# Performance work log

Hardware: AMD Instinct MI355X
Metric: run time of the kernel (lower is better)

Reference implementation:

```python
import jax, jax.numpy as jnp
import numpy as np

B, I, H = 16384, 512, 512


def _linear_params(key, out_dim, in_dim):
    kw, kb = jax.random.split(key)
    bound = 1.0 / np.sqrt(in_dim)
    W = jax.random.uniform(kw, (out_dim, in_dim), jnp.float32, -bound, bound)
    b = jax.random.uniform(kb, (out_dim,), jnp.float32, -bound, bound)
    return W, b


def setup_inputs() -> dict:
    key = jax.random.key(0)
    ks = jax.random.split(key, 12)
    x = jax.random.normal(ks[0], (B, I), jnp.float32)
    h_prev = jax.random.normal(ks[1], (B, H), jnp.float32)
    c_prev = jax.random.normal(ks[2], (B, H), jnp.float32)
    W_xi, b_xi = _linear_params(ks[3], H, I)
    W_hi, b_hi = _linear_params(ks[4], H, H)
    W_xf, b_xf = _linear_params(ks[5], H, I)
    W_hf, b_hf = _linear_params(ks[6], H, H)
    W_xc, b_xc = _linear_params(ks[7], H, I)
    W_hc, b_hc = _linear_params(ks[8], H, H)
    W_xo, b_xo = _linear_params(ks[9], H, I)
    W_ho, b_ho = _linear_params(ks[10], H, H)
    W_e, b_e = _linear_params(ks[11], H, I + H)
    return dict(x=x, h_prev=h_prev, c_prev=c_prev,
                W_xi=W_xi, b_xi=b_xi, W_hi=W_hi, b_hi=b_hi,
                W_xf=W_xf, b_xf=b_xf, W_hf=W_hf, b_hf=b_hf,
                W_xc=W_xc, b_xc=b_xc, W_hc=W_hc, b_hc=b_hc,
                W_xo=W_xo, b_xo=b_xo, W_ho=W_ho, b_ho=b_ho,
                W_e=W_e, b_e=b_e)


def reference(x, h_prev, c_prev,
              W_xi, b_xi, W_hi, b_hi,
              W_xf, b_xf, W_hf, b_hf,
              W_xc, b_xc, W_hc, b_hc,
              W_xo, b_xo, W_ho, b_ho,
              W_e, b_e):
    # Batch the 4 input-to-hidden projections into one GEMM and the 4
    # hidden-to-hidden projections into another (same math as 8 Linears).
    Wx = jnp.concatenate([W_xi, W_xf, W_xc, W_xo], axis=0)   # [4H, I]
    bx = jnp.concatenate([b_xi, b_xf, b_xc, b_xo], axis=0)   # [4H]
    Wh = jnp.concatenate([W_hi, W_hf, W_hc, W_ho], axis=0)   # [4H, H]
    bh = jnp.concatenate([b_hi, b_hf, b_hc, b_ho], axis=0)
    gates = (x @ Wx.T + bx) + (h_prev @ Wh.T + bh)            # [B, 4H]
    gi, gf, gc, go = jnp.split(gates, 4, axis=-1)
    i = jax.nn.sigmoid(gi)
    f = jax.nn.sigmoid(gf)
    g = jnp.tanh(gc)
    o = jax.nn.sigmoid(go)
    c = f * c_prev + i * g
    # exp gate: Linear on [x, h_prev] -> tanh -> exp; split W_e to avoid concat
    We_x, We_h = W_e[:, :x.shape[-1]], W_e[:, x.shape[-1]:]
    exp_factor = jnp.exp(jnp.tanh(x @ We_x.T + h_prev @ We_h.T + b_e))
    h = o * jnp.tanh(c) * exp_factor
    return (h, c)
```

## Files before the change

### kernel.cpp

```cpp
#include <hip/hip_runtime.h>
#include <stdint.h>

#define Bsz 16384
#define Hh  512
#define Kd  1024
#define BM  128
#define BNJ 32
#define BK  64
#define NT  16

#define LDSB 36864

typedef __attribute__((ext_vector_type(8))) short bf16x8;
typedef __attribute__((ext_vector_type(4))) float f32x4;
typedef __attribute__((ext_vector_type(8))) unsigned short u16x8;

__device__ __forceinline__ unsigned short f2bf(float f) {
    union { float f; unsigned u; } v; v.f = f;
    unsigned u = v.u;
    return (unsigned short)((u + 0x7fffu + ((u >> 16) & 1u)) >> 16);
}
__device__ __forceinline__ float fast_tanh(float x) {
    float e = __expf(2.f * x);
    return (e - 1.f) / (e + 1.f);
}
__device__ __forceinline__ float fast_sigmoid(float x) {
    return 1.f / (1.f + __expf(-x));
}

__global__ void pack_A(const float* __restrict__ x, const float* __restrict__ h,
                       unsigned short* __restrict__ A) {
    const long total = (long)Bsz * Kd / 8;
    for (long i = (long)blockIdx.x * blockDim.x + threadIdx.x; i < total;
         i += (long)gridDim.x * blockDim.x) {
        long row = i >> 7;
        int  col = ((int)(i & 127)) << 3;
        const float* src = (col < 512) ? (x + row * 512 + col)
                                       : (h + row * 512 + (col - 512));
        float4 f0 = *(const float4*)(src);
        float4 f1 = *(const float4*)(src + 4);
        u16x8 o;
        o[0]=f2bf(f0.x); o[1]=f2bf(f0.y); o[2]=f2bf(f0.z); o[3]=f2bf(f0.w);
        o[4]=f2bf(f1.x); o[5]=f2bf(f1.y); o[6]=f2bf(f1.z); o[7]=f2bf(f1.w);
        *(u16x8*)(A + (i << 3)) = o;
    }
}

__global__ void pack_B(const float* __restrict__ Wxi, const float* __restrict__ Whi,
                       const float* __restrict__ Wxf, const float* __restrict__ Whf,
                       const float* __restrict__ Wxc, const float* __restrict__ Whc,
                       const float* __restrict__ Wxo, const float* __restrict__ Who,
                       const float* __restrict__ We,
                       const float* __restrict__ bxi, const float* __restrict__ bhi,
                       const float* __restrict__ bxf, const float* __restrict__ bhf,
                       const float* __restrict__ bxc, const float* __restrict__ bhc,
                       const float* __restrict__ bxo, const float* __restrict__ bho,
                       const float* __restrict__ be,
                       unsigned short* __restrict__ Bp, float* __restrict__ bias) {
    const long id = (long)blockIdx.x * blockDim.x + threadIdx.x;
    if (id < 327680) {
        int blk = (int)(id >> 6);
        int l   = (int)(id & 63);
        int kh  = blk & 1;
        int kt  = (blk >> 1) & 15;
        int rest = blk >> 5;
        int g    = rest % 5;
        int jgrp = rest / 5;
        int j  = jgrp * 16 + (l & 15);
        int k0 = kt * 64 + kh * 32 + ((l >> 4) << 3);
        const float* src;
        if (g == 4) {
            src = We + (long)j * 1024 + k0;
        } else {
            const float* Wx = (g == 0) ? Wxi : (g == 1) ? Wxf : (g == 2) ? Wxc : Wxo;
            const float* Wh = (g == 0) ? Whi : (g == 1) ? Whf : (g == 2) ? Whc : Who;
            src = (k0 < 512) ? (Wx + (long)j * 512 + k0)
                             : (Wh + (long)j * 512 + (k0 - 512));
        }
        float4 f0 = *(const float4*)(src);
        float4 f1 = *(const float4*)(src + 4);
        u16x8 o;
        o[0]=f2bf(f0.x); o[1]=f2bf(f0.y); o[2]=f2bf(f0.z); o[3]=f2bf(f0.w);
        o[4]=f2bf(f1.x); o[5]=f2bf(f1.y); o[6]=f2bf(f1.z); o[7]=f2bf(f1.w);
        *(u16x8*)(Bp + (long)blk * 512 + l * 8) = o;
    }
    if (id < 2560) {
        int row = (int)id;
        int g = row >> 9, j = row & 511;
        float b;
        if (g == 4) b = be[j];
        else {
            const float* bx = (g == 0) ? bxi : (g == 1) ? bxf : (g == 2) ? bxc : bxo;
            const float* bh = (g == 0) ? bhi : (g == 1) ? bhf : (g == 2) ? bhc : bho;
            b = bx[j] + bh[j];
        }
        bias[row] = b;
    }
}

#define GL16(g, l) __builtin_amdgcn_global_load_lds( \
    (const __attribute__((address_space(1))) unsigned int*)(g), \
    (__attribute__((address_space(3))) unsigned int*)(l), 16, 0, 0)

#define WAITVM0()  asm volatile("s_waitcnt vmcnt(0)" ::: "memory")
#define LGKM_I(n)  asm volatile("s_waitcnt lgkmcnt(" #n ")" ::: "memory")
#define LGKM(n)    LGKM_I(n)
#define BARRIER()  asm volatile("s_barrier" ::: "memory")
#define SCHED0()   __builtin_amdgcn_sched_barrier(0)

#define MF(a, b, c) __builtin_amdgcn_mfma_f32_16x16x32_bf16(a, b, c, 0, 0, 0)

#define RDA(KH, APTR) do { \
    afA[KH][0] = *(const bf16x8*)((APTR) + 0 * 2048); \
    afA[KH][1] = *(const bf16x8*)((APTR) + 1 * 2048); \
    afA[KH][2] = *(const bf16x8*)((APTR) + 2 * 2048); \
    afA[KH][3] = *(const bf16x8*)((APTR) + 3 * 2048); \
} while (0)

#define RDB(SET, BPTR, KH) do { \
    SET[0] = *(const bf16x8*)((BPTR) + (0 + (KH)) * 1024); \
    SET[1] = *(const bf16x8*)((BPTR) + (2 + (KH)) * 1024); \
    SET[2] = *(const bf16x8*)((BPTR) + (4 + (KH)) * 1024); \
    SET[3] = *(const bf16x8*)((BPTR) + (6 + (KH)) * 1024); \
    SET[4] = *(const bf16x8*)((BPTR) + (8 + (KH)) * 1024); \
} while (0)

#define SGA(SO, T) do { \
    GL16(asrc + 0 * 32768 + (T) * 64, lds_raw + (SO) + adst + 0 * 4096); \
    GL16(asrc + 1 * 32768 + (T) * 64, lds_raw + (SO) + adst + 1 * 4096); \
    GL16(asrc + 2 * 32768 + (T) * 64, lds_raw + (SO) + adst + 2 * 4096); \
    GL16(asrc + 3 * 32768 + (T) * 64, lds_raw + (SO) + adst + 3 * 4096); \
} while (0)

#define SGB(SO, T) do { \
    GL16(bsg0 + (T) * 1024, lds_raw + (SO) + bdo0); \
    GL16(bsg1 + (T) * 1024, lds_raw + (SO) + bdo1); \
    GL16(bsg2 + (T) * 1024, lds_raw + (SO) + bdo2); \
    GL16(bsg3 + (T) * 1024, lds_raw + (SO) + bdo3); \
    GL16(bsg4 + (T) * 1024, lds_raw + (SO) + bdo4); \
} while (0)

#define MFMA20(KH, BSET) do { \
    __builtin_amdgcn_s_setprio(1); \
    _Pragma("unroll") \
    for (int g_ = 0; g_ < 5; ++g_) { \
        acc[g_][0] = MF(afA[KH][0], BSET[g_], acc[g_][0]); \
        acc[g_][1] = MF(afA[KH][1], BSET[g_], acc[g_][1]); \
        acc[g_][2] = MF(afA[KH][2], BSET[g_], acc[g_][2]); \
        acc[g_][3] = MF(afA[KH][3], BSET[g_], acc[g_][3]); \
    } \
    __builtin_amdgcn_s_setprio(0); \
} while (0)

#define TILE(AP0, AP1, BPTR, SO, T, STG, SYNC) do { \
    if (STG) { SGB(SO, (T) + 1); SGA(SO, (T) + 1); } SCHED0(); \
    RDA(0, AP0); RDB(bq0, BPTR, 0); SCHED0(); \
    RDA(1, AP1); RDB(bq1, BPTR, 1); SCHED0(); \
    LGKM(9); SCHED0(); \
    MFMA20(0, bq0); SCHED0(); \
    LGKM(0); SCHED0(); \
    MFMA20(1, bq1); \
    if (SYNC) { WAITVM0(); BARRIER(); } \
} while (0)

__global__ __launch_bounds__(256, 2)
void xlstm_gemm(const unsigned short* __restrict__ A,
                const unsigned short* __restrict__ Bp,
                const float* __restrict__ bias,
                const float* __restrict__ c_prev,
                float* __restrict__ out) {
    __shared__ __align__(16) unsigned char lds_raw[2 * LDSB];

    const int tid  = threadIdx.x;
    const int wid  = tid >> 6;
    const int lane = tid & 63;
    const int wm   = wid >> 1;
    const int wj   = wid & 1;
    const int fr   = lane & 15;
    const int q    = lane >> 4;

    const int orig = blockIdx.x;
    const int wg   = (orig & 7) * 256 + (orig >> 3);
    const int mblk = wg >> 4;
    const int jblk = wg & 15;
    const long brow = (long)mblk * BM;
    const int  bcol = jblk * BNJ;

    f32x4 acc[5][4];
#pragma unroll
    for (int g = 0; g < 5; ++g)
#pragma unroll
        for (int m = 0; m < 4; ++m)
#pragma unroll
            for (int r = 0; r < 4; ++r) acc[g][m][r] = 0.f;

    bf16x8 afA[2][4];
    bf16x8 bq0[5], bq1[5];

    const int aboff = (wm * 64 + fr) * 128;
    const int swz0  = ((q) ^ (fr & 7)) << 4;
    const int swz1  = ((4 | q) ^ (fr & 7)) << 4;
    const unsigned char* aP0k0 = lds_raw + aboff + swz0;
    const unsigned char* aP0k1 = lds_raw + aboff + swz1;
    const unsigned char* aP1k0 = aP0k0 + LDSB;
    const unsigned char* aP1k1 = aP0k1 + LDSB;
    const unsigned char* bP0 = lds_raw + 16384 + wj * 10240 + lane * 16;
    const unsigned char* bP1 = bP0 + LDSB;

    const int r0_ = tid >> 3;
    const unsigned short* asrc = A + (brow + r0_) * 1024L
                                   + (((tid & 7) ^ (r0_ & 7)) << 3);
    const int adst = tid * 16;
    const int f0_ = tid >> 6;
    const unsigned short *bsg0, *bsg1, *bsg2, *bsg3, *bsg4;
    int bdo0, bdo1, bdo2, bdo3, bdo4;
#define BSTG_INIT(i) do { \
    int f_ = f0_ + 4 * (i); int jl_ = f_ / 10; int rem_ = f_ - 10 * jl_; \
    bsg##i = Bp + (long)(jblk * 2 + jl_) * 81920 + (rem_ >> 1) * 16384 \
               + (rem_ & 1) * 512 + (tid & 63) * 8; \
    bdo##i = 16384 + jl_ * 10240 + rem_ * 1024 + (tid & 63) * 16; \
} while (0)
    BSTG_INIT(0); BSTG_INIT(1); BSTG_INIT(2); BSTG_INIT(3); BSTG_INIT(4);

    SGB(0, 0);
    SGA(0, 0);
    WAITVM0();
    BARRIER();

    for (int t = 0; t < 14; t += 2) {
        TILE(aP0k0, aP0k1, bP0, LDSB, t,     1, 1);
        TILE(aP1k0, aP1k1, bP1, 0,    t + 1, 1, 1);
    }
    TILE(aP0k0, aP0k1, bP0, LDSB, 14, 1, 1);
    TILE(aP1k0, aP1k1, bP1, 0,    15, 0, 0);

    const int j = bcol + wj * 16 + fr;
    const float bi_ = bias[j];
    const float bf_ = bias[512 + j];
    const float bc_ = bias[1024 + j];
    const float bo_ = bias[1536 + j];
    const float be_ = bias[2048 + j];
    const long mbase = brow + wm * 64 + (q << 2);
#pragma unroll
    for (int m = 0; m < 4; ++m) {
#pragma unroll
        for (int r = 0; r < 4; ++r) {
            long row = mbase + m * 16 + r;
            float gi = acc[0][m][r] + bi_;
            float gf = acc[1][m][r] + bf_;
            float gc = acc[2][m][r] + bc_;
            float go = acc[3][m][r] + bo_;
            float ge = acc[4][m][r] + be_;
            float iv = fast_sigmoid(gi);
            float fv = fast_sigmoid(gf);
            float gv = fast_tanh(gc);
            float ov = fast_sigmoid(go);
            float ef = __expf(fast_tanh(ge));
            float cp = c_prev[row * 512 + j];
            float cv = fv * cp + iv * gv;
            float hv = ov * fast_tanh(cv) * ef;
            out[row * 512 + j] = hv;
            out[(long)Bsz * 512 + row * 512 + j] = cv;
        }
    }
}

extern "C" void kernel_launch(void* const* d_in, const int* in_sizes, int n_in,
                              void* d_out, int out_size, void* d_ws, size_t ws_size,
                              hipStream_t stream) {
    const float* x      = (const float*)d_in[0];
    const float* h_prev = (const float*)d_in[1];
    const float* c_prev = (const float*)d_in[2];
    const float* Wxi = (const float*)d_in[3];
    const float* bxi = (const float*)d_in[4];
    const float* Whi = (const float*)d_in[5];
    const float* bhi = (const float*)d_in[6];
    const float* Wxf = (const float*)d_in[7];
    const float* bxf = (const float*)d_in[8];
    const float* Whf = (const float*)d_in[9];
    const float* bhf = (const float*)d_in[10];
    const float* Wxc = (const float*)d_in[11];
    const float* bxc = (const float*)d_in[12];
    const float* Whc = (const float*)d_in[13];
    const float* bhc = (const float*)d_in[14];
    const float* Wxo = (const float*)d_in[15];
    const float* bxo = (const float*)d_in[16];
    const float* Who = (const float*)d_in[17];
    const float* bho = (const float*)d_in[18];
    const float* We  = (const float*)d_in[19];
    const float* be  = (const float*)d_in[20];

    unsigned short* Abf  = (unsigned short*)d_ws;
    unsigned short* Bp   = (unsigned short*)((char*)d_ws + 33554432);
    float*          bias = (float*)((char*)d_ws + 33554432 + 5242880);

    pack_A<<<2048, 256, 0, stream>>>(x, h_prev, Abf);
    pack_B<<<1280, 256, 0, stream>>>(Wxi, Whi, Wxf, Whf, Wxc, Whc, Wxo, Who, We,
                                     bxi, bhi, bxf, bhf, bxc, bhc, bxo, bho, be,
                                     Bp, bias);
    xlstm_gemm<<<2048, 256, 0, stream>>>(Abf, Bp, bias, c_prev, (float*)d_out);
}
```

Measured before the change: 124.0 us.

## Restructure GEMM into 8-wave blocks with 4-buffer BK=32 LDS pipeline

The GEMM kernel now uses 512 threads per block (8 waves, each covering 32 rows instead of 64) with BK halved to 32, and a 4-stage LDS ring buffer in place of double buffering. Global-to-LDS loads are issued three tiles ahead with partial vmcnt waits, and LDS fragment reads for the next tile are double-buffered in registers so they overlap the current MFMAs. The aim is to hide memory latency and raise wave occupancy. In exchange there are twice as many barriers, and each wave does less MFMA work between syncs.

```diff
diff --git a/kernel.cpp b/kernel.cpp
--- a/kernel.cpp
+++ b/kernel.cpp
@@ -6,10 +6,10 @@
 #define Kd  1024
 #define BM  128
 #define BNJ 32
-#define BK  64
-#define NT  16
-
-#define LDSB 36864
+#define BK  32
+#define NT  32
+
+#define BUFB 18432
 
 typedef __attribute__((ext_vector_type(8))) short bf16x8;
 typedef __attribute__((ext_vector_type(4))) float f32x4;
@@ -102,7 +102,8 @@
     (const __attribute__((address_space(1))) unsigned int*)(g), \
     (__attribute__((address_space(3))) unsigned int*)(l), 16, 0, 0)
 
-#define WAITVM0()  asm volatile("s_waitcnt vmcnt(0)" ::: "memory")
+#define VM_I(n)    asm volatile("s_waitcnt vmcnt(" #n ")" ::: "memory")
+#define VM(n)      VM_I(n)
 #define LGKM_I(n)  asm volatile("s_waitcnt lgkmcnt(" #n ")" ::: "memory")
 #define LGKM(n)    LGKM_I(n)
 #define BARRIER()  asm volatile("s_barrier" ::: "memory")
@@ -110,66 +111,67 @@
 
 #define MF(a, b, c) __builtin_amdgcn_mfma_f32_16x16x32_bf16(a, b, c, 0, 0, 0)
 
-#define RDA(KH, APTR) do { \
-    afA[KH][0] = *(const bf16x8*)((APTR) + 0 * 2048); \
-    afA[KH][1] = *(const bf16x8*)((APTR) + 1 * 2048); \
-    afA[KH][2] = *(const bf16x8*)((APTR) + 2 * 2048); \
-    afA[KH][3] = *(const bf16x8*)((APTR) + 3 * 2048); \
-} while (0)
-
-#define RDB(SET, BPTR, KH) do { \
-    SET[0] = *(const bf16x8*)((BPTR) + (0 + (KH)) * 1024); \
-    SET[1] = *(const bf16x8*)((BPTR) + (2 + (KH)) * 1024); \
-    SET[2] = *(const bf16x8*)((BPTR) + (4 + (KH)) * 1024); \
-    SET[3] = *(const bf16x8*)((BPTR) + (6 + (KH)) * 1024); \
-    SET[4] = *(const bf16x8*)((BPTR) + (8 + (KH)) * 1024); \
-} while (0)
-
-#define SGA(SO, T) do { \
-    GL16(asrc + 0 * 32768 + (T) * 64, lds_raw + (SO) + adst + 0 * 4096); \
-    GL16(asrc + 1 * 32768 + (T) * 64, lds_raw + (SO) + adst + 1 * 4096); \
-    GL16(asrc + 2 * 32768 + (T) * 64, lds_raw + (SO) + adst + 2 * 4096); \
-    GL16(asrc + 3 * 32768 + (T) * 64, lds_raw + (SO) + adst + 3 * 4096); \
-} while (0)
-
-#define SGB(SO, T) do { \
-    GL16(bsg0 + (T) * 1024, lds_raw + (SO) + bdo0); \
-    GL16(bsg1 + (T) * 1024, lds_raw + (SO) + bdo1); \
-    GL16(bsg2 + (T) * 1024, lds_raw + (SO) + bdo2); \
-    GL16(bsg3 + (T) * 1024, lds_raw + (SO) + bdo3); \
-    GL16(bsg4 + (T) * 1024, lds_raw + (SO) + bdo4); \
-} while (0)
-
-#define MFMA20(KH, BSET) do { \
+#define RD7(S, BO) do { \
+    q##S##0 = *(const bf16x8*)(bP + (BO) + 0 * 1024); \
+    q##S##1 = *(const bf16x8*)(bP + (BO) + 1 * 1024); \
+    q##S##2 = *(const bf16x8*)(bP + (BO) + 2 * 1024); \
+    q##S##3 = *(const bf16x8*)(bP + (BO) + 3 * 1024); \
+    q##S##4 = *(const bf16x8*)(bP + (BO) + 4 * 1024); \
+    a##S##0 = *(const bf16x8*)(aP + (BO) + 0 * 1024); \
+    a##S##1 = *(const bf16x8*)(aP + (BO) + 1 * 1024); \
+} while (0)
+
+#define MFMA10(S) do { \
     __builtin_amdgcn_s_setprio(1); \
-    _Pragma("unroll") \
-    for (int g_ = 0; g_ < 5; ++g_) { \
-        acc[g_][0] = MF(afA[KH][0], BSET[g_], acc[g_][0]); \
-        acc[g_][1] = MF(afA[KH][1], BSET[g_], acc[g_][1]); \
-        acc[g_][2] = MF(afA[KH][2], BSET[g_], acc[g_][2]); \
-        acc[g_][3] = MF(afA[KH][3], BSET[g_], acc[g_][3]); \
+    acc[0][0] = MF(a##S##0, q##S##0, acc[0][0]); \
+    acc[0][1] = MF(a##S##1, q##S##0, acc[0][1]); \
+    acc[1][0] = MF(a##S##0, q##S##1, acc[1][0]); \
+    acc[1][1] = MF(a##S##1, q##S##1, acc[1][1]); \
+    acc[2][0] = MF(a##S##0, q##S##2, acc[2][0]); \
+    acc[2][1] = MF(a##S##1, q##S##2, acc[2][1]); \
+    acc[3][0] = MF(a##S##0, q##S##3, acc[3][0]); \
+    acc[3][1] = MF(a##S##1, q##S##3, acc[3][1]); \
+    acc[4][0] = MF(a##S##0, q##S##4, acc[4][0]); \
+    acc[4][1] = MF(a##S##1, q##S##4, acc[4][1]); \
+    __builtin_amdgcn_s_setprio(0); \
+} while (0)
+
+#define SG3(BO, T) do { \
+    GL16(sg0 + (long)(T) * st0, lds_raw + (BO) + sd0); \
+    GL16(sg1 + (long)(T) * st1, lds_raw + (BO) + sd1); \
+    GL16(sg2 + (long)(T) * st2, lds_raw + (BO) + sd2); \
+} while (0)
+
+#define TILE_F(T, SC, SN, RBO, SBO, STG, SYNC, WN) do { \
+    if (STG) SG3(SBO, (T) + 3); \
+    RD7(SN, RBO); \
+    LGKM(7); SCHED0(); \
+    MFMA10(SC); \
+    if (SYNC) { VM(WN); BARRIER(); } \
+} while (0)
+
+#define SLOT_INIT(i) do { \
+    int u_ = wid * 3 + (i); if (u_ >= 18) u_ -= 18; \
+    if (u_ < 8) { \
+        int row_ = u_ * 16 + (lane >> 2); \
+        sg##i = A + (brow + row_) * 1024L \
+                  + (((lane & 3) ^ ((row_ >> 1) & 3)) << 3); \
+        st##i = 32; \
+    } else { \
+        int b_ = u_ - 8; int jl_ = b_ / 5; int g_ = b_ - 5 * jl_; \
+        sg##i = Bp + (long)(jblk * 2 + jl_) * 81920 + g_ * 16384 + lane * 8; \
+        st##i = 512; \
     } \
-    __builtin_amdgcn_s_setprio(0); \
-} while (0)
-
-#define TILE(AP0, AP1, BPTR, SO, T, STG, SYNC) do { \
-    if (STG) { SGB(SO, (T) + 1); SGA(SO, (T) + 1); } SCHED0(); \
-    RDA(0, AP0); RDB(bq0, BPTR, 0); SCHED0(); \
-    RDA(1, AP1); RDB(bq1, BPTR, 1); SCHED0(); \
-    LGKM(9); SCHED0(); \
-    MFMA20(0, bq0); SCHED0(); \
-    LGKM(0); SCHED0(); \
-    MFMA20(1, bq1); \
-    if (SYNC) { WAITVM0(); BARRIER(); } \
-} while (0)
-
-__global__ __launch_bounds__(256, 2)
+    sd##i = u_ * 1024 + lane * 16; \
+} while (0)
+
+__global__ __launch_bounds__(512, 4)
 void xlstm_gemm(const unsigned short* __restrict__ A,
                 const unsigned short* __restrict__ Bp,
                 const float* __restrict__ bias,
                 const float* __restrict__ c_prev,
                 float* __restrict__ out) {
-    __shared__ __align__(16) unsigned char lds_raw[2 * LDSB];
+    __shared__ __align__(16) unsigned char lds_raw[4 * BUFB];
 
     const int tid  = threadIdx.x;
     const int wid  = tid >> 6;
@@ -186,53 +188,43 @@
     const long brow = (long)mblk * BM;
     const int  bcol = jblk * BNJ;
 
-    f32x4 acc[5][4];
+    f32x4 acc[5][2];
 #pragma unroll
     for (int g = 0; g < 5; ++g)
 #pragma unroll
-        for (int m = 0; m < 4; ++m)
+        for (int m = 0; m < 2; ++m)
 #pragma unroll
             for (int r = 0; r < 4; ++r) acc[g][m][r] = 0.f;
 
-    bf16x8 afA[2][4];
-    bf16x8 bq0[5], bq1[5];
-
-    const int aboff = (wm * 64 + fr) * 128;
-    const int swz0  = ((q) ^ (fr & 7)) << 4;
-    const int swz1  = ((4 | q) ^ (fr & 7)) << 4;
-    const unsigned char* aP0k0 = lds_raw + aboff + swz0;
-    const unsigned char* aP0k1 = lds_raw + aboff + swz1;
-    const unsigned char* aP1k0 = aP0k0 + LDSB;
-    const unsigned char* aP1k1 = aP0k1 + LDSB;
-    const unsigned char* bP0 = lds_raw + 16384 + wj * 10240 + lane * 16;
-    const unsigned char* bP1 = bP0 + LDSB;
-
-    const int r0_ = tid >> 3;
-    const unsigned short* asrc = A + (brow + r0_) * 1024L
-                                   + (((tid & 7) ^ (r0_ & 7)) << 3);
-    const int adst = tid * 16;
-    const int f0_ = tid >> 6;
-    const unsigned short *bsg0, *bsg1, *bsg2, *bsg3, *bsg4;
-    int bdo0, bdo1, bdo2, bdo3, bdo4;
-#define BSTG_INIT(i) do { \
-    int f_ = f0_ + 4 * (i); int jl_ = f_ / 10; int rem_ = f_ - 10 * jl_; \
-    bsg##i = Bp + (long)(jblk * 2 + jl_) * 81920 + (rem_ >> 1) * 16384 \
-               + (rem_ & 1) * 512 + (tid & 63) * 8; \
-    bdo##i = 16384 + jl_ * 10240 + rem_ * 1024 + (tid & 63) * 16; \
-} while (0)
-    BSTG_INIT(0); BSTG_INIT(1); BSTG_INIT(2); BSTG_INIT(3); BSTG_INIT(4);
-
-    SGB(0, 0);
-    SGA(0, 0);
-    WAITVM0();
+    bf16x8 qA0, qA1, qA2, qA3, qA4, aA0, aA1;
+    bf16x8 qB0, qB1, qB2, qB3, qB4, aB0, aB1;
+
+    const unsigned char* aP = lds_raw + wm * 2048 + fr * 64
+                              + ((q ^ ((fr >> 1) & 3)) << 4);
+    const unsigned char* bP = lds_raw + 8192 + wj * 5120 + lane * 16;
+
+    const unsigned short *sg0, *sg1, *sg2;
+    int st0, st1, st2, sd0, sd1, sd2;
+    SLOT_INIT(0); SLOT_INIT(1); SLOT_INIT(2);
+
+    SG3(0 * BUFB, 0);
+    SG3(1 * BUFB, 1);
+    SG3(2 * BUFB, 2);
+    VM(3);
     BARRIER();
-
-    for (int t = 0; t < 14; t += 2) {
-        TILE(aP0k0, aP0k1, bP0, LDSB, t,     1, 1);
-        TILE(aP1k0, aP1k1, bP1, 0,    t + 1, 1, 1);
-    }
-    TILE(aP0k0, aP0k1, bP0, LDSB, 14, 1, 1);
-    TILE(aP1k0, aP1k1, bP1, 0,    15, 0, 0);
+    RD7(A, 0 * BUFB);
+
+    for (int t = 0; t < 28; t += 4) {
+        TILE_F(t + 0, A, B, 1 * BUFB, 3 * BUFB, 1, 1, 3);
+        TILE_F(t + 1, B, A, 2 * BUFB, 0 * BUFB, 1, 1, 3);
+        TILE_F(t + 2, A, B, 3 * BUFB, 1 * BUFB, 1, 1, 3);
+        TILE_F(t + 3, B, A, 0 * BUFB, 2 * BUFB, 1, 1, 3);
+    }
+    TILE_F(28, A, B, 1 * BUFB, 3 * BUFB, 1, 1, 3);
+    TILE_F(29, B, A, 2 * BUFB, 0,        0, 1, 0);
+    TILE_F(30, A, B, 3 * BUFB, 0,        0, 0, 0);
+    LGKM(0); SCHED0();
+    MFMA10(B);
 
     const int j = bcol + wj * 16 + fr;
     const float bi_ = bias[j];
@@ -240,9 +232,9 @@
     const float bc_ = bias[1024 + j];
     const float bo_ = bias[1536 + j];
     const float be_ = bias[2048 + j];
-    const long mbase = brow + wm * 64 + (q << 2);
-#pragma unroll
-    for (int m = 0; m < 4; ++m) {
+    const long mbase = brow + wm * 32 + (q << 2);
+#pragma unroll
+    for (int m = 0; m < 2; ++m) {
 #pragma unroll
         for (int r = 0; r < 4; ++r) {
             long row = mbase + m * 16 + r;
@@ -298,5 +290,5 @@
     pack_B<<<1280, 256, 0, stream>>>(Wxi, Whi, Wxf, Whf, Wxc, Whc, Wxo, Who, We,
                                      bxi, bhi, bxf, bhf, bxc, bhc, bxo, bho, be,
                                      Bp, bias);
-    xlstm_gemm<<<2048, 256, 0, stream>>>(Abf, Bp, bias, c_prev, (float*)d_out);
-}
+    xlstm_gemm<<<2048, 512, 0, stream>>>(Abf, Bp, bias, c_prev, (float*)d_out);
+}
```

After: 267.7 us. 116% more time.
